# Performance work log

Hardware: AMD Instinct MI355X
Metric: run time of the kernel (lower is better)

## Reference

```python
import jax, jax.numpy as jnp
import numpy as np

N = 100000      # total nodes across batch of graphs
E = 1600000     # total edges (avg degree 16)
DIN = 16        # raw node feature dim
H = 128         # social_hidden_dim
HEADS = 4
DOUT = H // HEADS
LAYERS = 2
G = 64          # number of graphs in batch
FOUT = 256      # fusion_hidden_dim
NEG_SLOPE = 0.2


def layer_norm(x, g, b, eps=1e-5):
    mu = x.mean(-1, keepdims=True)
    var = ((x - mu) ** 2).mean(-1, keepdims=True)
    return (x - mu) / jnp.sqrt(var + eps) * g + b


def gat_conv(h, src, dst, W, a_src, a_dst, bias):
    # h: [N,H]; src/dst: [E+N] (self-loops included)
    hp = (h @ W).reshape(N, HEADS, DOUT)                    # [N,heads,dout]
    al_s = jnp.einsum('nhd,hd->nh', hp, a_src)              # [N,heads]
    al_d = jnp.einsum('nhd,hd->nh', hp, a_dst)
    logits = jax.nn.leaky_relu(al_s[src] + al_d[dst], NEG_SLOPE)  # [Etot,heads]
    m = jax.ops.segment_max(logits, dst, num_segments=N)    # segment softmax over dst
    e = jnp.exp(logits - m[dst])
    denom = jax.ops.segment_sum(e, dst, num_segments=N)
    alpha = e / (denom[dst] + 1e-16)                        # [Etot,heads]
    msg = hp[src] * alpha[:, :, None]                       # [Etot,heads,dout]
    out = jax.ops.segment_sum(msg, dst, num_segments=N)     # scatter-add
    return out.reshape(N, H) + bias


def setup_inputs():
    key = jax.random.key(0)
    ks = jax.random.split(key, 24)
    s = 0.05
    inp = {
        'x': jax.random.normal(ks[0], (N, DIN), jnp.float32),
        'edge_index': jax.random.randint(ks[1], (2, E), 0, N, jnp.int32),
        'node2graph': (jnp.arange(N, dtype=jnp.int32) * G // N).astype(jnp.int32),
        'Wp': jax.random.normal(ks[2], (DIN, H)) * s,
        'bp': jnp.zeros((H,)),
        'Wq1': jax.random.normal(ks[3], (2 * H, H)) * s,
        'bq1': jnp.zeros((H,)),
        'gq': jnp.ones((H,)), 'beq': jnp.zeros((H,)),
        'Wq2': jax.random.normal(ks[4], (H, FOUT)) * s,
        'bq2': jnp.zeros((FOUT,)),
    }
    for i in range(LAYERS):
        inp[f'Wg{i}'] = jax.random.normal(ks[5 + 4 * i], (H, H)) * s
        inp[f'as{i}'] = jax.random.normal(ks[6 + 4 * i], (HEADS, DOUT)) * s
        inp[f'ad{i}'] = jax.random.normal(ks[7 + 4 * i], (HEADS, DOUT)) * s
        inp[f'bg{i}'] = jnp.zeros((H,))
        inp[f'g{i}'] = jnp.ones((H,))
        inp[f'be{i}'] = jnp.zeros((H,))
    return inp


def reference(x, edge_index, node2graph, Wp, bp, Wq1, bq1, gq, beq, Wq2, bq2,
              Wg0, as0, ad0, bg0, g0, be0, Wg1, as1, ad1, bg1, g1, be1):
    loop = jnp.arange(N, dtype=edge_index.dtype)
    src = jnp.concatenate([edge_index[0], loop])  # add self-loops (PyG default)
    dst = jnp.concatenate([edge_index[1], loop])

    h = jax.nn.gelu(x @ Wp + bp, approximate=False)
    params = [(Wg0, as0, ad0, bg0, g0, be0), (Wg1, as1, ad1, bg1, g1, be1)]
    for (W, a_s, a_d, b, g, be) in params:
        h_new = gat_conv(h, src, dst, W, a_s, a_d, b)
        h = layer_norm(h_new + h, g, be)  # dims match -> residual

    counts = jax.ops.segment_sum(jnp.ones((N, 1), h.dtype), node2graph, num_segments=G)
    mean_pool = jax.ops.segment_sum(h, node2graph, num_segments=G) / jnp.maximum(counts, 1.0)
    max_pool = jax.ops.segment_max(h, node2graph, num_segments=G)
    emb = jnp.concatenate([mean_pool, max_pool], axis=-1)  # [G, 2H]

    p = layer_norm(emb @ Wq1 + bq1, gq, beq)
    p = jax.nn.gelu(p, approximate=False)
    return p @ Wq2 + bq2  # [G, FOUT]
```

## Files before the change

### kernel.cpp

```cpp
#include <hip/hip_runtime.h>

typedef unsigned short u16;
typedef unsigned char u8;
typedef unsigned int u32;
typedef unsigned long long u64;
typedef short short8 __attribute__((ext_vector_type(8)));
typedef float f32x4 __attribute__((ext_vector_type(4)));
typedef float f32x2 __attribute__((ext_vector_type(2)));

#define NN   100000
#define EE   1600000
#define NG   64
#define WSTR 136
#define NB   196
#define BSHIFT 9
#define BMASK 511
#define BCAP 12288
#define OCAP 262144
#define EPB  4096

constexpr size_t AL256(size_t x) { return (x + 255) & ~(size_t)255; }
constexpr size_t OFF_FLAG   = 0;
constexpr size_t OFF_OCNT   = AL256(OFF_FLAG + 256);
constexpr size_t OFF_BCNT   = AL256(OFF_OCNT + 256 * 4);
constexpr size_t OFF_ROWPTR = AL256(OFF_BCNT + 256 * 4);
constexpr size_t OFF_DEG    = AL256(OFF_ROWPTR + (size_t)(NN + 1) * 4);
constexpr size_t OFF_COL    = AL256(OFF_DEG + (size_t)NN * 4);
constexpr size_t OFF_ALS    = AL256(OFF_COL + (size_t)(EE + 1024) * 4);
constexpr size_t OFF_ALD    = AL256(OFF_ALS + (size_t)NN * 4 * 4);
constexpr size_t OFF_GSUM   = AL256(OFF_ALD + (size_t)NN * 4 * 4);
constexpr size_t OFF_GKEY   = AL256(OFF_GSUM + (size_t)NG * 128 * 4);
constexpr size_t OFF_GCNT   = AL256(OFF_GKEY + (size_t)NG * 128 * 4);
constexpr size_t OFF_H      = AL256(OFF_GCNT + (size_t)NG * 4);
constexpr size_t OFF_HPB    = AL256(OFF_H + (size_t)NN * 128 * 2);
constexpr size_t OFF_EBUF   = AL256(OFF_HPB + (size_t)NN * 128 * 1);
constexpr size_t OFF_OBUF   = AL256(OFF_EBUF + (size_t)NB * BCAP * 4);
constexpr size_t WS_TOTAL   = AL256(OFF_OBUF + (size_t)OCAP * 8);

__device__ u64 g_ws[WS_TOTAL / 8];

__device__ __forceinline__ char* wsp() { return (char*)g_ws; }
#define WS_FLAG   ((int*)(wsp() + OFF_FLAG))
#define WS_OCNT   ((int*)(wsp() + OFF_OCNT))
#define WS_BCNT   ((int*)(wsp() + OFF_BCNT))
#define WS_ROWPTR ((int*)(wsp() + OFF_ROWPTR))
#define WS_DEG    ((int*)(wsp() + OFF_DEG))
#define WS_COL    ((int*)(wsp() + OFF_COL))
#define WS_ALS    ((float*)(wsp() + OFF_ALS))
#define WS_ALD    ((float*)(wsp() + OFF_ALD))
#define WS_GSUM   ((float*)(wsp() + OFF_GSUM))
#define WS_GKEY   ((u32*)(wsp() + OFF_GKEY))
#define WS_GCNT   ((int*)(wsp() + OFF_GCNT))
#define WS_H      ((u16*)(wsp() + OFF_H))
#define WS_HPB    ((u8*)(wsp() + OFF_HPB))
#define WS_EBUF   ((u32*)(wsp() + OFF_EBUF))
#define WS_OBUF   ((u64*)(wsp() + OFF_OBUF))

__device__ __forceinline__ float b2f(u16 u) { return __uint_as_float(((u32)u) << 16); }
__device__ __forceinline__ float b2f_lo(u32 u) { return __uint_as_float(u << 16); }
__device__ __forceinline__ float b2f_hi(u32 u) { return __uint_as_float(u & 0xffff0000u); }
__device__ __forceinline__ u16 f2bf(float f) {
    u32 u = __float_as_uint(f);
    return (u16)((u + 0x7fffu + ((u >> 16) & 1u)) >> 16);
}
__device__ __forceinline__ float ldf(const void* p, int i, int bf) {
    return bf ? b2f(((const u16*)p)[i]) : ((const float*)p)[i];
}
__device__ __forceinline__ int ldint(const int* p, long long i, int wide) {
    return wide ? p[i * 2] : p[(size_t)i];
}
__device__ __forceinline__ u32 fkey(float f) {
    u32 u = __float_as_uint(f);
    return (u >> 31) ? ~u : (u | 0x80000000u);
}
__device__ __forceinline__ float funkey(u32 k) {
    u32 u = (k & 0x80000000u) ? (k & 0x7fffffffu) : ~k;
    return __uint_as_float(u);
}

__global__ __launch_bounds__(256) void k_zero(const void* __restrict__ x,
                                              const int* __restrict__ ei) {
    if (blockIdx.x == 0 && threadIdx.x < 64) {
        int t = threadIdx.x;
        const u16* p = (const u16*)x;
        u16 u = p[t * 2];
        int e = (u >> 7) & 0xff;
        int ok = ((u & 0x7fffu) == 0) || (e >= 0x60 && e <= 0x9f);
        u64 m1 = __ballot(ok);
        int z = (ei[t * 2 + 1] == 0);
        u64 m2 = __ballot(z);
        if (t == 0) {
            WS_FLAG[0] = (__popcll(m1) >= 48) ? 1 : 0;
            WS_FLAG[1] = (__popcll(m2) >= 56) ? 1 : 0;
        }
    }
    if (blockIdx.x == 0 && threadIdx.x == 64) WS_FLAG[2] = 0;
    int i = blockIdx.x * 256 + threadIdx.x;
    if (i < NN) WS_DEG[i] = 0;
    if (i < NG * 128) { WS_GSUM[i] = 0.f; WS_GKEY[i] = 0u; }
    if (i < NG) WS_GCNT[i] = 0;
    if (i < NB) { WS_BCNT[i] = 0; WS_OCNT[i] = 0; }
}

__global__ __launch_bounds__(256) void k_bucket(const int* __restrict__ ei) {
    __shared__ int lcnt[NB], lbase[NB], lcur[NB];
    int t = threadIdx.x;
    int wide = WS_FLAG[1];
    for (int i = t; i < NB; i += 256) { lcnt[i] = 0; lcur[i] = 0; }
    __syncthreads();
    int e0 = blockIdx.x * EPB + t;
    int sA[16], dA[16];
#pragma unroll
    for (int j = 0; j < 16; j++) {
        int e = e0 + j * 256;
        int s = -1, d = 0;
        if (e < EE) {
            if (wide) { s = ((const int2*)ei)[e].x; d = ((const int2*)ei)[(size_t)EE + e].x; }
            else      { s = ei[e];                  d = ei[(size_t)EE + e]; }
            if ((u32)s >= NN || (u32)d >= NN) s = -1;
        }
        sA[j] = s; dA[j] = d;
        if (s >= 0) atomicAdd(&lcnt[d >> BSHIFT], 1);
    }
    __syncthreads();
    for (int i = t; i < NB; i += 256)
        lbase[i] = atomicAdd(&WS_BCNT[i], lcnt[i]);
    __syncthreads();
    u32* ebuf = WS_EBUF;
#pragma unroll
    for (int j = 0; j < 16; j++) {
        int s = sA[j], d = dA[j];
        if (s < 0) continue;
        int b = d >> BSHIFT;
        int r = atomicAdd(&lcur[b], 1);
        int slot = lbase[b] + r;
        if (slot < BCAP) {
            ebuf[(size_t)b * BCAP + slot] = ((u32)(d & BMASK) << 17) | (u32)s;
        } else {
            int o = atomicAdd(&WS_FLAG[2], 1);
            if (o < OCAP) {
                WS_OBUF[o] = ((u64)(u32)d << 32) | (u32)s;
                atomicAdd(&WS_DEG[d], 1);
                atomicAdd(&WS_OCNT[d >> BSHIFT], 1);
            }
        }
    }
}

__global__ __launch_bounds__(512) void k_place() {
    __shared__ int hist[512];
    __shared__ int sbase[256];
    __shared__ int bws[4];
    __shared__ int wsum[8];
    int b = blockIdx.x, t = threadIdx.x;
    int lane = t & 63, wv = t >> 6;
    hist[t] = 0;
    if (t < 256) {
        int c = 0;
        if (t < NB) {
            c = WS_BCNT[t]; if (c > BCAP) c = BCAP;
            c += WS_OCNT[t];
        }
        int x = c;
#pragma unroll
        for (int off = 1; off < 64; off <<= 1) {
            int y = __shfl_up(x, off);
            if (lane >= off) x += y;
        }
        if (lane == 63) bws[wv] = x;
        sbase[t] = x;
    }
    __syncthreads();
    if (t == 0) {
        int a = 0;
#pragma unroll
        for (int i = 0; i < 4; i++) { int tmp = bws[i]; bws[i] = a; a += tmp; }
    }
    __syncthreads();
    if (t < 256) sbase[t] += bws[t >> 6];
    __syncthreads();
    int base = (b > 0) ? sbase[b - 1] : 0;
    if (b == 0 && t == 0) WS_ROWPTR[NN] = sbase[NB - 1];
    int bc = WS_BCNT[b]; if (bc > BCAP) bc = BCAP;
    const u32* eb = WS_EBUF + (size_t)b * BCAP;
    for (int i = t; i < bc; i += 512)
        atomicAdd(&hist[eb[i] >> 17], 1);
    __syncthreads();
    int n = (b << BSHIFT) + t;
    int v = (n < NN) ? (hist[t] + WS_DEG[n]) : 0;
    int x = v;
#pragma unroll
    for (int off = 1; off < 64; off <<= 1) {
        int y = __shfl_up(x, off);
        if (lane >= off) x += y;
    }
    if (lane == 63) wsum[wv] = x;
    __syncthreads();
    if (wv == 0 && lane < 8) {
        int y = wsum[lane];
#pragma unroll
        for (int off = 1; off < 8; off <<= 1) {
            int z = __shfl_up(y, off);
            if (lane >= off) y += z;
        }
        wsum[lane] = y;
    }
    __syncthreads();
    int r = base + x + (wv > 0 ? wsum[wv - 1] : 0) - v;
    if (n < NN) WS_ROWPTR[n] = r;
    __syncthreads();
    hist[t] = r;
    __syncthreads();
    for (int i = t; i < bc; i += 512) {
        u32 pk = eb[i];
        int pos = atomicAdd(&hist[pk >> 17], 1);
        WS_COL[pos] = (int)(pk & 0x1ffffu);
    }
    int cnt = WS_FLAG[2]; if (cnt > OCAP) cnt = OCAP;
    for (int i = t; i < cnt; i += 512) {
        u64 pk = WS_OBUF[i];
        int d = (int)(pk >> 32);
        if ((d >> BSHIFT) == b) {
            int pos = atomicAdd(&hist[d & BMASK], 1);
            WS_COL[pos] = (int)(pk & 0xffffffffu);
        }
    }
}

__global__ __launch_bounds__(128) void k_proj(const void* __restrict__ x,
                                              const void* __restrict__ Wp,
                                              const void* __restrict__ bp) {
    __shared__ float sW[16 * 128];
    int t = threadIdx.x;
    int bf = WS_FLAG[0];
    for (int i = t; i < 16 * 128; i += 128) sW[i] = ldf(Wp, i, bf);
    __syncthreads();
    float bj = ldf(bp, t, bf);
    for (int n = blockIdx.x; n < NN; n += gridDim.x) {
        float acc = bj;
#pragma unroll
        for (int k = 0; k < 16; k++)
            acc = fmaf(ldf(x, n * 16 + k, bf), sW[k * 128 + t], acc);
        float g = 0.5f * acc * (1.0f + erff(acc * 0.70710678118654752f));
        WS_H[(size_t)n * 128 + t] = f2bf(g);
    }
}

__global__ __launch_bounds__(256) void k_gemm(const void* __restrict__ Wg,
                                              const void* __restrict__ a_s,
                                              const void* __restrict__ a_d) {
    __shared__ __align__(16) u16 sWt[128 * WSTR];
    __shared__ __align__(16) u16 sH[32 * WSTR];
    int t = threadIdx.x;
    int bf = WS_FLAG[0];
    for (int idx = t; idx < 128 * 128; idx += 256) {
        int k = idx >> 7, n = idx & 127;
        sWt[n * WSTR + k] = bf ? ((const u16*)Wg)[idx] : f2bf(((const float*)Wg)[idx]);
    }
    __syncthreads();
    int wv = t >> 6, lane = t & 63;
    int n0 = wv * 32;
    int quad = lane >> 4, m16 = lane & 15;
    int ce = n0 + 2 * m16;
    float as0v = ldf(a_s, ce, bf),     as1v = ldf(a_s, ce + 1, bf);
    float ad0v = ldf(a_d, ce, bf),     ad1v = ldf(a_d, ce + 1, bf);
    short8 bfr[2][4];
#pragma unroll
    for (int nt = 0; nt < 2; nt++) {
        int n = ce + nt;
#pragma unroll
        for (int ks = 0; ks < 4; ks++)
            bfr[nt][ks] = *(const short8*)&sWt[n * WSTR + ks * 32 + quad * 8];
    }
    u8* hp = WS_HPB;
    const u32* h32 = (const u32*)WS_H;
    u32* sH32 = (u32*)sH;
    for (int m0 = blockIdx.x * 32; m0 < NN; m0 += gridDim.x * 32) {
        __syncthreads();
        for (int idx = t; idx < 32 * 64; idx += 256) {
            int r = idx >> 6, c2 = idx & 63;
            sH32[r * 68 + c2] = h32[(size_t)(m0 + r) * 64 + c2];
        }
        __syncthreads();
#pragma unroll
        for (int sub = 0; sub < 2; sub++) {
            f32x4 acc0 = {0.f, 0.f, 0.f, 0.f};
            f32x4 acc1 = {0.f, 0.f, 0.f, 0.f};
#pragma unroll
            for (int ks = 0; ks < 4; ks++) {
                short8 af = *(const short8*)&sH[(sub * 16 + m16) * WSTR + ks * 32 + quad * 8];
                acc0 = __builtin_amdgcn_mfma_f32_16x16x32_bf16(af, bfr[0][ks], acc0, 0, 0, 0);
                acc1 = __builtin_amdgcn_mfma_f32_16x16x32_bf16(af, bfr[1][ks], acc1, 0, 0, 0);
            }
            int mbase = m0 + sub * 16;
#pragma unroll
            for (int r = 0; r < 4; r++) {
                size_t row = (size_t)(mbase + quad * 4 + r) * 128;
                u32 pk8 = (u32)__builtin_amdgcn_cvt_pk_fp8_f32(acc0[r], acc1[r], 0, false);
                *(u16*)&hp[row + ce] = (u16)(pk8 & 0xffffu);
                float ps = acc0[r] * as0v + acc1[r] * as1v;
                float pd = acc0[r] * ad0v + acc1[r] * ad1v;
#pragma unroll
                for (int m = 1; m <= 8; m <<= 1) {
                    ps += __shfl_xor(ps, m);
                    pd += __shfl_xor(pd, m);
                }
                if (m16 == 0) {
                    int nrow = mbase + quad * 4 + r;
                    WS_ALS[nrow * 4 + wv] = ps;
                    WS_ALD[nrow * 4 + wv] = pd;
                }
            }
        }
    }
}

__global__ __launch_bounds__(512) void k_gat(const void* __restrict__ bg,
                                             const void* __restrict__ gam,
                                             const void* __restrict__ bet) {
    int wid = threadIdx.x >> 6, lane = threadIdx.x & 63;
    int n = blockIdx.x * 8 + wid;
    if (n >= NN) return;
    int bf = WS_FLAG[0];
    const int* col = WS_COL;
    const float* als = WS_ALS;
    int k0 = WS_ROWPTR[n], deg = WS_ROWPTR[n + 1] - k0;
    int hd = lane >> 4, eo = lane & 15;
    float aldh = WS_ALD[n * 4 + hd];
    const u16* hp16 = (const u16*)WS_HPB;
    u32* h32 = (u32*)WS_H;
    u32 hv = h32[(size_t)n * 64 + lane];
    u16 pvs = hp16[(size_t)n * 64 + lane];
    int base48 = lane & 48;

    float vs = als[n * 4 + hd] + aldh;
    vs = vs > 0.f ? vs : 0.2f * vs;
    float wself = __expf(vs);

    int i0 = eo, i1 = eo + 16;
    int e0 = k0 + (i0 < deg ? i0 : 0);
    int e1 = k0 + (i1 < deg ? i1 : 0);
    int sc0 = col[e0];
    int sc1 = col[e1];
    if ((u32)sc0 >= NN) sc0 = 0;
    if ((u32)sc1 >= NN) sc1 = 0;
    float v0 = als[sc0 * 4 + hd] + aldh;
    float v1 = als[sc1 * 4 + hd] + aldh;
    v0 = v0 > 0.f ? v0 : 0.2f * v0;
    v1 = v1 > 0.f ? v1 : 0.2f * v1;
    float w0 = (i0 < deg) ? __expf(v0) : 0.f;
    float w1 = (i1 < deg) ? __expf(v1) : 0.f;
    float se = w0 + w1;
    f32x2 mvs = __builtin_amdgcn_cvt_pk_f32_fp8((int)pvs, false);
    float a0 = wself * mvs.x, a1 = wself * mvs.y;

#pragma unroll
    for (int j = 0; j < 16; j++) {
        float wj = __shfl(w0, base48 + j);
        int   sj = __builtin_amdgcn_readlane(sc0, j);
        u16 pv = hp16[(size_t)sj * 64 + lane];
        f32x2 mv = __builtin_amdgcn_cvt_pk_f32_fp8((int)pv, false);
        a0 = fmaf(wj, mv.x, a0);
        a1 = fmaf(wj, mv.y, a1);
    }
    if (deg > 16) {
#pragma unroll
        for (int j = 0; j < 16; j++) {
            float wj = __shfl(w1, base48 + j);
            int   sj = __builtin_amdgcn_readlane(sc1, j);
            u16 pv = hp16[(size_t)sj * 64 + lane];
            f32x2 mv = __builtin_amdgcn_cvt_pk_f32_fp8((int)pv, false);
            a0 = fmaf(wj, mv.x, a0);
            a1 = fmaf(wj, mv.y, a1);
        }
    }

    if (__builtin_expect(deg > 32, 0)) {
        for (int c = 32; c < deg; c += 16) {
            int i = c + eo;
            float w = 0.f; int scol = 0;
            if (i < deg) {
                scol = col[k0 + i];
                float v = als[scol * 4 + hd] + aldh;
                v = v > 0.f ? v : 0.2f * v;
                w = __expf(v);
            }
            se += w;
            int rem = deg - c; if (rem > 16) rem = 16;
            for (int j = 0; j < rem; j++) {
                float wj = __shfl(w, base48 + j);
                int sj = __shfl(scol, base48 + j);
                u16 pv = hp16[(size_t)sj * 64 + lane];
                f32x2 mv = __builtin_amdgcn_cvt_pk_f32_fp8((int)pv, false);
                a0 = fmaf(wj, mv.x, a0);
                a1 = fmaf(wj, mv.y, a1);
            }
        }
    }

    se += __shfl_xor(se, 1);
    se += __shfl_xor(se, 2);
    se += __shfl_xor(se, 4);
    se += __shfl_xor(se, 8);
    se += wself;
    float inv = 1.f / (se + 1e-16f);
    int d0 = lane * 2, d1 = d0 + 1;
    float r0 = a0 * inv + ldf(bg, d0, bf) + b2f_lo(hv);
    float r1 = a1 * inv + ldf(bg, d1, bf) + b2f_hi(hv);
    float s1 = r0 + r1;
#pragma unroll
    for (int m = 1; m <= 32; m <<= 1) s1 += __shfl_xor(s1, m);
    float mu = s1 * (1.f / 128.f);
    float e0f = r0 - mu, e1f = r1 - mu;
    float s2 = e0f * e0f + e1f * e1f;
#pragma unroll
    for (int m = 1; m <= 32; m <<= 1) s2 += __shfl_xor(s2, m);
    float rstd = rsqrtf(s2 * (1.f / 128.f) + 1e-5f);
    float y0 = e0f * rstd * ldf(gam, d0, bf) + ldf(bet, d0, bf);
    float y1 = e1f * rstd * ldf(gam, d1, bf) + ldf(bet, d1, bf);
    h32[(size_t)n * 64 + lane] = (u32)f2bf(y0) | ((u32)f2bf(y1) << 16);
}

__global__ __launch_bounds__(128) void k_pool(const int* __restrict__ n2g) {
    int j = threadIdx.x;
    int wide = WS_FLAG[1];
    int n0 = blockIdx.x * 128;
    int n1 = n0 + 128; if (n1 > NN) n1 = NN;
    float runs = 0.f, runm = -3.4e38f;
    int rung = -1, runc = 0;
    for (int n = n0; n < n1; n++) {
        int g = ldint(n2g, n, wide);
        if (g != rung) {
            if (rung >= 0 && (u32)rung < NG) {
                atomicAdd(&WS_GSUM[rung * 128 + j], runs);
                atomicMax(&WS_GKEY[rung * 128 + j], fkey(runm));
                if (j == 0) atomicAdd(&WS_GCNT[rung], runc);
            }
            rung = g; runs = 0.f; runm = -3.4e38f; runc = 0;
        }
        float v = b2f(WS_H[(size_t)n * 128 + j]);
        runs += v;
        runm = fmaxf(runm, v);
        runc++;
    }
    if (rung >= 0 && (u32)rung < NG) {
        atomicAdd(&WS_GSUM[rung * 128 + j], runs);
        atomicMax(&WS_GKEY[rung * 128 + j], fkey(runm));
        if (j == 0) atomicAdd(&WS_GCNT[rung], runc);
    }
}

__global__ __launch_bounds__(256) void k_head(const void* __restrict__ Wq1,
                                              const void* __restrict__ bq1,
                                              const void* __restrict__ gq,
                                              const void* __restrict__ beq,
                                              const void* __restrict__ Wq2,
                                              const void* __restrict__ bq2,
                                              float* __restrict__ out) {
    __shared__ float sem[256];
    __shared__ float sp2[256];
    __shared__ float sp[128];
    __shared__ float red[4];
    int g = blockIdx.x, t = threadIdx.x;
    int bf = WS_FLAG[0];
    float cnt = fmaxf((float)WS_GCNT[g], 1.f);
    if (t < 128) sem[t] = WS_GSUM[g * 128 + t] / cnt;
    else         sem[t] = funkey(WS_GKEY[g * 128 + (t - 128)]);
    __syncthreads();
    {
        int half = t >> 7, o = t & 127;
        float acc = half ? 0.f : ldf(bq1, o, bf);
        int kb = half * 128;
        for (int k = kb; k < kb + 128; k++)
            acc = fmaf(sem[k], ldf(Wq1, k * 128 + o, bf), acc);
        sp2[t] = acc;
    }
    __syncthreads();
    float a = 0.f;
    if (t < 128) a = sp2[t] + sp2[t + 128];
    int lane = t & 63, wv = t >> 6;
    float s1 = (t < 128) ? a : 0.f;
#pragma unroll
    for (int m = 1; m <= 32; m <<= 1) s1 += __shfl_xor(s1, m);
    if (lane == 0) red[wv] = s1;
    __syncthreads();
    float mu = (red[0] + red[1]) * (1.f / 128.f);
    float d = (t < 128) ? (a - mu) : 0.f;
    float s2 = d * d;
#pragma unroll
    for (int m = 1; m <= 32; m <<= 1) s2 += __shfl_xor(s2, m);
    __syncthreads();
    if (lane == 0) red[wv] = s2;
    __syncthreads();
    float var = (red[0] + red[1]) * (1.f / 128.f);
    if (t < 128) {
        float p = d * rsqrtf(var + 1e-5f) * ldf(gq, t, bf) + ldf(beq, t, bf);
        sp[t] = 0.5f * p * (1.0f + erff(p * 0.70710678118654752f));
    }
    __syncthreads();
    float o = ldf(bq2, t, bf);
    for (int k = 0; k < 128; k++)
        o = fmaf(sp[k], ldf(Wq2, k * 256 + t, bf), o);
    out[g * 256 + t] = o;
}

extern "C" void kernel_launch(void* const* d_in, const int* in_sizes, int n_in,
                              void* d_out, int out_size, void* d_ws, size_t ws_size,
                              hipStream_t stream) {
    const void* x   = d_in[0];
    const int* ei   = (const int*)d_in[1];
    const int* n2g  = (const int*)d_in[2];
    const void* Wp  = d_in[3];
    const void* bp  = d_in[4];
    const void* Wq1 = d_in[5];
    const void* bq1 = d_in[6];
    const void* gq  = d_in[7];
    const void* beq = d_in[8];
    const void* Wq2 = d_in[9];
    const void* bq2 = d_in[10];
    const void* Wg0 = d_in[11];
    const void* as0 = d_in[12];
    const void* ad0 = d_in[13];
    const void* bg0 = d_in[14];
    const void* g0  = d_in[15];
    const void* be0 = d_in[16];
    const void* Wg1 = d_in[17];
    const void* as1 = d_in[18];
    const void* ad1 = d_in[19];
    const void* bg1 = d_in[20];
    const void* g1  = d_in[21];
    const void* be1 = d_in[22];
    (void)d_ws; (void)ws_size; (void)in_sizes; (void)n_in; (void)out_size;

    k_zero<<<(NN + 255) / 256, 256, 0, stream>>>(x, ei);

    k_bucket<<<(EE + EPB - 1) / EPB, 256, 0, stream>>>(ei);
    k_place<<<NB, 512, 0, stream>>>();

    k_proj<<<2048, 128, 0, stream>>>(x, Wp, bp);

    k_gemm<<<768, 256, 0, stream>>>(Wg0, as0, ad0);
    k_gat<<<(NN + 7) / 8, 512, 0, stream>>>(bg0, g0, be0);
    k_gemm<<<768, 256, 0, stream>>>(Wg1, as1, ad1);
    k_gat<<<(NN + 7) / 8, 512, 0, stream>>>(bg1, g1, be1);

    k_pool<<<(NN + 127) / 128, 128, 0, stream>>>(n2g);
    k_head<<<NG, 256, 0, stream>>>(Wq1, bq1, gq, beq, Wq2, bq2, (float*)d_out);
}
```

Before: 523.8 us.

## Co-schedule edge bucketing with projection and CSR placement with first GEMM

Merges the edge bucketing kernel and the input projection into one launch, with block ranges picking the role, and does the same for CSR placement and the layer-0 GEMM. Shared memory is reused through unions. The independent stages can then overlap on the GPU, and two kernel launch boundaries go away. The GEMM is also reorganized to 512 threads, with 8 waves each taking one head and one 16-row half of the tile. This costs larger blocks and a possibly different occupancy for the GEMM.

```diff
diff --git a/kernel.cpp b/kernel.cpp
--- a/kernel.cpp
+++ b/kernel.cpp
@@ -18,6 +18,10 @@
 #define BCAP 12288
 #define OCAP 262144
 #define EPB  4096
+#define NBK  391
+#define NPJ  1024
+#define KBP  196
+#define KBG  384
 
 constexpr size_t AL256(size_t x) { return (x + 255) & ~(size_t)255; }
 constexpr size_t OFF_FLAG   = 0;
@@ -102,57 +106,144 @@
     if (i < NB) { WS_BCNT[i] = 0; WS_OCNT[i] = 0; }
 }
 
-__global__ __launch_bounds__(256) void k_bucket(const int* __restrict__ ei) {
-    __shared__ int lcnt[NB], lbase[NB], lcur[NB];
+__global__ __launch_bounds__(256) void k_bucket_proj(const int* __restrict__ ei,
+                                                     const void* __restrict__ x,
+                                                     const void* __restrict__ Wp,
+                                                     const void* __restrict__ bp) {
+    __shared__ union {
+        struct { int lcnt[NB], lbase[NB], lcur[NB]; } b;
+        float sW[16 * 128];
+    } sm;
     int t = threadIdx.x;
-    int wide = WS_FLAG[1];
-    for (int i = t; i < NB; i += 256) { lcnt[i] = 0; lcur[i] = 0; }
-    __syncthreads();
-    int e0 = blockIdx.x * EPB + t;
-    int sA[16], dA[16];
-#pragma unroll
-    for (int j = 0; j < 16; j++) {
-        int e = e0 + j * 256;
-        int s = -1, d = 0;
-        if (e < EE) {
-            if (wide) { s = ((const int2*)ei)[e].x; d = ((const int2*)ei)[(size_t)EE + e].x; }
-            else      { s = ei[e];                  d = ei[(size_t)EE + e]; }
-            if ((u32)s >= NN || (u32)d >= NN) s = -1;
-        }
-        sA[j] = s; dA[j] = d;
-        if (s >= 0) atomicAdd(&lcnt[d >> BSHIFT], 1);
-    }
-    __syncthreads();
-    for (int i = t; i < NB; i += 256)
-        lbase[i] = atomicAdd(&WS_BCNT[i], lcnt[i]);
-    __syncthreads();
-    u32* ebuf = WS_EBUF;
-#pragma unroll
-    for (int j = 0; j < 16; j++) {
-        int s = sA[j], d = dA[j];
-        if (s < 0) continue;
-        int b = d >> BSHIFT;
-        int r = atomicAdd(&lcur[b], 1);
-        int slot = lbase[b] + r;
-        if (slot < BCAP) {
-            ebuf[(size_t)b * BCAP + slot] = ((u32)(d & BMASK) << 17) | (u32)s;
-        } else {
-            int o = atomicAdd(&WS_FLAG[2], 1);
-            if (o < OCAP) {
-                WS_OBUF[o] = ((u64)(u32)d << 32) | (u32)s;
-                atomicAdd(&WS_DEG[d], 1);
-                atomicAdd(&WS_OCNT[d >> BSHIFT], 1);
-            }
-        }
-    }
-}
-
-__global__ __launch_bounds__(512) void k_place() {
-    __shared__ int hist[512];
-    __shared__ int sbase[256];
-    __shared__ int bws[4];
-    __shared__ int wsum[8];
-    int b = blockIdx.x, t = threadIdx.x;
+    if (blockIdx.x < NBK) {
+        int wide = WS_FLAG[1];
+        for (int i = t; i < NB; i += 256) { sm.b.lcnt[i] = 0; sm.b.lcur[i] = 0; }
+        __syncthreads();
+        int e0 = blockIdx.x * EPB + t;
+        int sA[16], dA[16];
+#pragma unroll
+        for (int j = 0; j < 16; j++) {
+            int e = e0 + j * 256;
+            int s = -1, d = 0;
+            if (e < EE) {
+                if (wide) { s = ((const int2*)ei)[e].x; d = ((const int2*)ei)[(size_t)EE + e].x; }
+                else      { s = ei[e];                  d = ei[(size_t)EE + e]; }
+                if ((u32)s >= NN || (u32)d >= NN) s = -1;
+            }
+            sA[j] = s; dA[j] = d;
+            if (s >= 0) atomicAdd(&sm.b.lcnt[d >> BSHIFT], 1);
+        }
+        __syncthreads();
+        for (int i = t; i < NB; i += 256)
+            sm.b.lbase[i] = atomicAdd(&WS_BCNT[i], sm.b.lcnt[i]);
+        __syncthreads();
+        u32* ebuf = WS_EBUF;
+#pragma unroll
+        for (int j = 0; j < 16; j++) {
+            int s = sA[j], d = dA[j];
+            if (s < 0) continue;
+            int b = d >> BSHIFT;
+            int r = atomicAdd(&sm.b.lcur[b], 1);
+            int slot = sm.b.lbase[b] + r;
+            if (slot < BCAP) {
+                ebuf[(size_t)b * BCAP + slot] = ((u32)(d & BMASK) << 17) | (u32)s;
+            } else {
+                int o = atomicAdd(&WS_FLAG[2], 1);
+                if (o < OCAP) {
+                    WS_OBUF[o] = ((u64)(u32)d << 32) | (u32)s;
+                    atomicAdd(&WS_DEG[d], 1);
+                    atomicAdd(&WS_OCNT[d >> BSHIFT], 1);
+                }
+            }
+        }
+    } else {
+        int pb = blockIdx.x - NBK;
+        int bf = WS_FLAG[0];
+        for (int i = t; i < 16 * 128; i += 256) sm.sW[i] = ldf(Wp, i, bf);
+        __syncthreads();
+        int half = t >> 7, j = t & 127;
+        float bj = ldf(bp, j, bf);
+        for (int pr = pb; pr < NN / 2; pr += NPJ) {
+            int n = pr * 2 + half;
+            float acc = bj;
+#pragma unroll
+            for (int k = 0; k < 16; k++)
+                acc = fmaf(ldf(x, n * 16 + k, bf), sm.sW[k * 128 + j], acc);
+            float g = 0.5f * acc * (1.0f + erff(acc * 0.70710678118654752f));
+            WS_H[(size_t)n * 128 + j] = f2bf(g);
+        }
+    }
+}
+
+__device__ __forceinline__ void gemm_body(int bid, int grid,
+                                          const void* __restrict__ Wg,
+                                          const void* __restrict__ a_s,
+                                          const void* __restrict__ a_d,
+                                          u16* sWt, u16* sH) {
+    int t = threadIdx.x;
+    int bf = WS_FLAG[0];
+    for (int idx = t; idx < 128 * 128; idx += 512) {
+        int k = idx >> 7, n = idx & 127;
+        sWt[n * WSTR + k] = bf ? ((const u16*)Wg)[idx] : f2bf(((const float*)Wg)[idx]);
+    }
+    __syncthreads();
+    int wv8 = t >> 6, lane = t & 63;
+    int head = wv8 & 3, sub = wv8 >> 2;
+    int n0 = head * 32;
+    int quad = lane >> 4, m16 = lane & 15;
+    int ce = n0 + 2 * m16;
+    float as0v = ldf(a_s, ce, bf),     as1v = ldf(a_s, ce + 1, bf);
+    float ad0v = ldf(a_d, ce, bf),     ad1v = ldf(a_d, ce + 1, bf);
+    short8 bfr[2][4];
+#pragma unroll
+    for (int nt = 0; nt < 2; nt++) {
+        int n = ce + nt;
+#pragma unroll
+        for (int ks = 0; ks < 4; ks++)
+            bfr[nt][ks] = *(const short8*)&sWt[n * WSTR + ks * 32 + quad * 8];
+    }
+    u8* hp = WS_HPB;
+    const u32* h32 = (const u32*)WS_H;
+    u32* sH32 = (u32*)sH;
+    for (int m0 = bid * 32; m0 < NN; m0 += grid * 32) {
+        __syncthreads();
+        for (int idx = t; idx < 32 * 64; idx += 512) {
+            int r = idx >> 6, c2 = idx & 63;
+            sH32[r * 68 + c2] = h32[(size_t)(m0 + r) * 64 + c2];
+        }
+        __syncthreads();
+        f32x4 acc0 = {0.f, 0.f, 0.f, 0.f};
+        f32x4 acc1 = {0.f, 0.f, 0.f, 0.f};
+#pragma unroll
+        for (int ks = 0; ks < 4; ks++) {
+            short8 af = *(const short8*)&sH[(sub * 16 + m16) * WSTR + ks * 32 + quad * 8];
+            acc0 = __builtin_amdgcn_mfma_f32_16x16x32_bf16(af, bfr[0][ks], acc0, 0, 0, 0);
+            acc1 = __builtin_amdgcn_mfma_f32_16x16x32_bf16(af, bfr[1][ks], acc1, 0, 0, 0);
+        }
+        int mbase = m0 + sub * 16;
+#pragma unroll
+        for (int r = 0; r < 4; r++) {
+            size_t row = (size_t)(mbase + quad * 4 + r) * 128;
+            u32 pk8 = (u32)__builtin_amdgcn_cvt_pk_fp8_f32(acc0[r], acc1[r], 0, false);
+            *(u16*)&hp[row + ce] = (u16)(pk8 & 0xffffu);
+            float ps = acc0[r] * as0v + acc1[r] * as1v;
+            float pd = acc0[r] * ad0v + acc1[r] * ad1v;
+#pragma unroll
+            for (int m = 1; m <= 8; m <<= 1) {
+                ps += __shfl_xor(ps, m);
+                pd += __shfl_xor(pd, m);
+            }
+            if (m16 == 0) {
+                int nrow = mbase + quad * 4 + r;
+                WS_ALS[nrow * 4 + head] = ps;
+                WS_ALD[nrow * 4 + head] = pd;
+            }
+        }
+    }
+}
+
+__device__ __forceinline__ void place_body(int b, int* hist, int* sbase, int* bws, int* wsum) {
+    int t = threadIdx.x;
     int lane = t & 63, wv = t >> 6;
     hist[t] = 0;
     if (t < 256) {
@@ -227,92 +318,26 @@
     }
 }
 
-__global__ __launch_bounds__(128) void k_proj(const void* __restrict__ x,
-                                              const void* __restrict__ Wp,
-                                              const void* __restrict__ bp) {
-    __shared__ float sW[16 * 128];
-    int t = threadIdx.x;
-    int bf = WS_FLAG[0];
-    for (int i = t; i < 16 * 128; i += 128) sW[i] = ldf(Wp, i, bf);
-    __syncthreads();
-    float bj = ldf(bp, t, bf);
-    for (int n = blockIdx.x; n < NN; n += gridDim.x) {
-        float acc = bj;
-#pragma unroll
-        for (int k = 0; k < 16; k++)
-            acc = fmaf(ldf(x, n * 16 + k, bf), sW[k * 128 + t], acc);
-        float g = 0.5f * acc * (1.0f + erff(acc * 0.70710678118654752f));
-        WS_H[(size_t)n * 128 + t] = f2bf(g);
-    }
-}
-
-__global__ __launch_bounds__(256) void k_gemm(const void* __restrict__ Wg,
+__global__ __launch_bounds__(512) void k_place_gemm(const void* __restrict__ Wg,
+                                                    const void* __restrict__ a_s,
+                                                    const void* __restrict__ a_d) {
+    __shared__ __align__(16) union {
+        struct { u16 sWt[128 * WSTR]; u16 sH[32 * WSTR]; } g;
+        struct { int hist[512]; int sbase[256]; int bws[4]; int wsum[8]; } p;
+    } sm;
+    if (blockIdx.x < KBP) {
+        place_body(blockIdx.x, sm.p.hist, sm.p.sbase, sm.p.bws, sm.p.wsum);
+    } else {
+        gemm_body(blockIdx.x - KBP, KBG, Wg, a_s, a_d, sm.g.sWt, sm.g.sH);
+    }
+}
+
+__global__ __launch_bounds__(512) void k_gemm(const void* __restrict__ Wg,
                                               const void* __restrict__ a_s,
                                               const void* __restrict__ a_d) {
     __shared__ __align__(16) u16 sWt[128 * WSTR];
     __shared__ __align__(16) u16 sH[32 * WSTR];
-    int t = threadIdx.x;
-    int bf = WS_FLAG[0];
-    for (int idx = t; idx < 128 * 128; idx += 256) {
-        int k = idx >> 7, n = idx & 127;
-        sWt[n * WSTR + k] = bf ? ((const u16*)Wg)[idx] : f2bf(((const float*)Wg)[idx]);
-    }
-    __syncthreads();
-    int wv = t >> 6, lane = t & 63;
-    int n0 = wv * 32;
-    int quad = lane >> 4, m16 = lane & 15;
-    int ce = n0 + 2 * m16;
-    float as0v = ldf(a_s, ce, bf),     as1v = ldf(a_s, ce + 1, bf);
-    float ad0v = ldf(a_d, ce, bf),     ad1v = ldf(a_d, ce + 1, bf);
-    short8 bfr[2][4];
-#pragma unroll
-    for (int nt = 0; nt < 2; nt++) {
-        int n = ce + nt;
-#pragma unroll
-        for (int ks = 0; ks < 4; ks++)
-            bfr[nt][ks] = *(const short8*)&sWt[n * WSTR + ks * 32 + quad * 8];
-    }
-    u8* hp = WS_HPB;
-    const u32* h32 = (const u32*)WS_H;
-    u32* sH32 = (u32*)sH;
-    for (int m0 = blockIdx.x * 32; m0 < NN; m0 += gridDim.x * 32) {
-        __syncthreads();
-        for (int idx = t; idx < 32 * 64; idx += 256) {
-            int r = idx >> 6, c2 = idx & 63;
-            sH32[r * 68 + c2] = h32[(size_t)(m0 + r) * 64 + c2];
-        }
-        __syncthreads();
-#pragma unroll
-        for (int sub = 0; sub < 2; sub++) {
-            f32x4 acc0 = {0.f, 0.f, 0.f, 0.f};
-            f32x4 acc1 = {0.f, 0.f, 0.f, 0.f};
-#pragma unroll
-            for (int ks = 0; ks < 4; ks++) {
-                short8 af = *(const short8*)&sH[(sub * 16 + m16) * WSTR + ks * 32 + quad * 8];
-                acc0 = __builtin_amdgcn_mfma_f32_16x16x32_bf16(af, bfr[0][ks], acc0, 0, 0, 0);
-                acc1 = __builtin_amdgcn_mfma_f32_16x16x32_bf16(af, bfr[1][ks], acc1, 0, 0, 0);
-            }
-            int mbase = m0 + sub * 16;
-#pragma unroll
-            for (int r = 0; r < 4; r++) {
-                size_t row = (size_t)(mbase + quad * 4 + r) * 128;
-                u32 pk8 = (u32)__builtin_amdgcn_cvt_pk_fp8_f32(acc0[r], acc1[r], 0, false);
-                *(u16*)&hp[row + ce] = (u16)(pk8 & 0xffffu);
-                float ps = acc0[r] * as0v + acc1[r] * as1v;
-                float pd = acc0[r] * ad0v + acc1[r] * ad1v;
-#pragma unroll
-                for (int m = 1; m <= 8; m <<= 1) {
-                    ps += __shfl_xor(ps, m);
-                    pd += __shfl_xor(pd, m);
-                }
-                if (m16 == 0) {
-                    int nrow = mbase + quad * 4 + r;
-                    WS_ALS[nrow * 4 + wv] = ps;
-                    WS_ALD[nrow * 4 + wv] = pd;
-                }
-            }
-        }
-    }
+    gemm_body(blockIdx.x, gridDim.x, Wg, a_s, a_d, sWt, sH);
 }
 
 __global__ __launch_bounds__(512) void k_gat(const void* __restrict__ bg,
@@ -534,14 +559,11 @@
 
     k_zero<<<(NN + 255) / 256, 256, 0, stream>>>(x, ei);
 
-    k_bucket<<<(EE + EPB - 1) / EPB, 256, 0, stream>>>(ei);
-    k_place<<<NB, 512, 0, stream>>>();
-
-    k_proj<<<2048, 128, 0, stream>>>(x, Wp, bp);
-
-    k_gemm<<<768, 256, 0, stream>>>(Wg0, as0, ad0);
+    k_bucket_proj<<<NBK + NPJ, 256, 0, stream>>>(ei, x, Wp, bp);
+    k_place_gemm<<<KBP + KBG, 512, 0, stream>>>(Wg0, as0, ad0);
+
     k_gat<<<(NN + 7) / 8, 512, 0, stream>>>(bg0, g0, be0);
-    k_gemm<<<768, 256, 0, stream>>>(Wg1, as1, ad1);
+    k_gemm<<<768, 512, 0, stream>>>(Wg1, as1, ad1);
     k_gat<<<(NN + 7) / 8, 512, 0, stream>>>(bg1, g1, be1);
 
     k_pool<<<(NN + 127) / 128, 128, 0, stream>>>(n2g);
```

Result: faster. 464.7 us (median of 2 runs) (-11.3%).
